# Kernel tuning notes

Measured on AMD Instinct MI355X. Metric: run time of the kernel, lower is better.

## Reference

```python
import jax, jax.numpy as jnp
import numpy as np

INF = 1e10
B, T, D, N, H = 4, 1024, 1024, 16, 4096
SCALE = float(np.sqrt(D))  # Attention built with d_key = d_model in original code


def _linear(x, w, b):
    return x @ w.T + b


def _layernorm(x, gamma, beta, eps=1e-6):
    # torch x.std(-1) is unbiased (ddof=1); eps added to std, matching original
    m = x.mean(-1, keepdims=True)
    var = ((x - m) ** 2).sum(-1, keepdims=True) / (x.shape[-1] - 1)
    return gamma * (x - m) / (jnp.sqrt(var) + eps) + beta


def _mha(q_in, k_in, v_in, wq, bq, wk, bk, wv, bv, wo, bo, mask, causal):
    Bb, Tq, Dm = q_in.shape
    Tk = k_in.shape[1]
    dh = Dm // N
    q = _linear(q_in, wq, bq).reshape(Bb, Tq, N, dh).transpose(0, 2, 1, 3)  # b n q d
    k = _linear(k_in, wk, bk).reshape(Bb, Tk, N, dh).transpose(0, 2, 1, 3)
    v = _linear(v_in, wv, bv).reshape(Bb, Tk, N, dh).transpose(0, 2, 1, 3)
    dots = jnp.einsum('bnqd,bnkd->bnqk', q, k)
    if causal and Tq == Tk:
        tri = jnp.triu(jnp.ones((Tq, Tk), dots.dtype), 1) * INF
        dots = dots - tri
    dots = dots - (1.0 - mask)[:, None, None, :] * INF  # mask: 1=keep
    probs = jax.nn.softmax(dots / SCALE, axis=-1)
    out = jnp.einsum('bnqk,bnkd->bnqd', probs, v)
    out = out.transpose(0, 2, 1, 3).reshape(Bb, Tq, Dm)
    return _linear(out, wo, bo)


def setup_inputs() -> dict:
    key = jax.random.key(0)
    ks = jax.random.split(key, 16)
    g = lambda k, shp: (jax.random.normal(k, shp, dtype=jnp.float32) * 0.02)
    inp = {
        'x': jax.random.normal(ks[0], (B, T, D), dtype=jnp.float32),
        'encoding': jax.random.normal(ks[1], (B, T, D), dtype=jnp.float32),
        'mask_src': jnp.ones((B, T), dtype=jnp.float32),
        'mask_trg': jnp.ones((B, T), dtype=jnp.float32),
        # causal self-attention projections
        'sa_wq': g(ks[2], (D, D)), 'sa_bq': jnp.zeros((D,), jnp.float32),
        'sa_wk': g(ks[3], (D, D)), 'sa_bk': jnp.zeros((D,), jnp.float32),
        'sa_wv': g(ks[4], (D, D)), 'sa_bv': jnp.zeros((D,), jnp.float32),
        'sa_wo': g(ks[5], (D, D)), 'sa_bo': jnp.zeros((D,), jnp.float32),
        'sa_gamma': jnp.ones((D,), jnp.float32), 'sa_beta': jnp.zeros((D,), jnp.float32),
        # cross-attention projections
        'ca_wq': g(ks[6], (D, D)), 'ca_bq': jnp.zeros((D,), jnp.float32),
        'ca_wk': g(ks[7], (D, D)), 'ca_bk': jnp.zeros((D,), jnp.float32),
        'ca_wv': g(ks[8], (D, D)), 'ca_bv': jnp.zeros((D,), jnp.float32),
        'ca_wo': g(ks[9], (D, D)), 'ca_bo': jnp.zeros((D,), jnp.float32),
        'ca_gamma': jnp.ones((D,), jnp.float32), 'ca_beta': jnp.zeros((D,), jnp.float32),
        # feedforward
        'ff_w1': g(ks[10], (H, D)), 'ff_b1': jnp.zeros((H,), jnp.float32),
        'ff_w2': g(ks[11], (D, H)), 'ff_b2': jnp.zeros((D,), jnp.float32),
        'ff_gamma': jnp.ones((D,), jnp.float32), 'ff_beta': jnp.zeros((D,), jnp.float32),
    }
    return inp


def reference(x, encoding, mask_src, mask_trg,
              sa_wq, sa_bq, sa_wk, sa_bk, sa_wv, sa_bv, sa_wo, sa_bo, sa_gamma, sa_beta,
              ca_wq, ca_bq, ca_wk, ca_bk, ca_wv, ca_bv, ca_wo, ca_bo, ca_gamma, ca_beta,
              ff_w1, ff_b1, ff_w2, ff_b2, ff_gamma, ff_beta):
    # DecoderLayer forward (eval: dropout = identity)
    h = _layernorm(x + _mha(x, x, x, sa_wq, sa_bq, sa_wk, sa_bk, sa_wv, sa_bv,
                            sa_wo, sa_bo, mask_trg, causal=True), sa_gamma, sa_beta)
    h = _layernorm(h + _mha(h, encoding, encoding, ca_wq, ca_bq, ca_wk, ca_bk,
                            ca_wv, ca_bv, ca_wo, ca_bo, mask_src, causal=False),
                   ca_gamma, ca_beta)
    ff = _linear(jax.nn.relu(_linear(h, ff_w1, ff_b1)), ff_w2, ff_b2)
    return _layernorm(h + ff, ff_gamma, ff_beta)
```

## Files before the change

kernel.cpp:

```cpp
#include <hip/hip_runtime.h>
#include <hip/hip_bf16.h>
#include <math.h>
#include <stdint.h>

#define BATCH   4
#define TSEQ    1024
#define DMODEL  1024
#define NHEAD   16
#define DHEAD   64
#define HFF     4096
#define MROWS   (BATCH * TSEQ)

typedef _Float16 f16;
typedef __attribute__((ext_vector_type(2))) _Float16 f16x2;
typedef __attribute__((ext_vector_type(4))) _Float16 f16x4;
typedef __attribute__((ext_vector_type(8))) _Float16 f16x8;
typedef __attribute__((ext_vector_type(4))) float    f32x4;

__global__ __launch_bounds__(256)
void cvt_f32_f16(const float* __restrict__ in, f16* __restrict__ out, int n)
{
    const int i = (blockIdx.x * 256 + threadIdx.x) * 8;
    if (i < n) {
        const float4 a = *(const float4*)(in + i);
        const float4 b = *(const float4*)(in + i + 4);
        f16x8 o;
        o[0] = (_Float16)a.x; o[1] = (_Float16)a.y; o[2] = (_Float16)a.z; o[3] = (_Float16)a.w;
        o[4] = (_Float16)b.x; o[5] = (_Float16)b.y; o[6] = (_Float16)b.z; o[7] = (_Float16)b.w;
        *(f16x8*)(out + i) = o;
    }
}

template<int TN, bool RES, bool RELU>
__global__ __launch_bounds__(256, 2)
void hgemm(const f16* __restrict__ A, const f16* __restrict__ Wt,
           const float* __restrict__ bias, const f16* __restrict__ Rm,
           f16* __restrict__ C, int M, int N, int K)
{
    constexpr int TM = 128, TK = 32;
    constexpr int NB = TN / 32;
    constexpr int AISS = (TM * TK) / (256 * 8);
    constexpr int BISS = (TN * TK) / (256 * 8);
    __shared__ alignas(16) f16 As[2][TM * TK];
    __shared__ alignas(16) f16 Bs[2][TN * TK];

    const int t = threadIdx.x, ln = t & 63, wv = t >> 6;
    const int wr = wv >> 1, wc = wv & 1;

    const int gx = gridDim.x;
    const int nbk = gx * gridDim.y;
    const int d  = blockIdx.y * gx + blockIdx.x;
    const int wid = (d & 7) * (nbk >> 3) + (d >> 3);
    const int bx = wid % gx, by = wid / gx;

    const size_t m0 = (size_t)by * TM, n0 = (size_t)bx * TN;

    f32x4 acc[4][NB];
#pragma unroll
    for (int i = 0; i < 4; ++i)
#pragma unroll
        for (int j = 0; j < NB; ++j) acc[i][j] = (f32x4){0.f, 0.f, 0.f, 0.f};

    const f16* Ag = A + (m0 + (t >> 2)) * (size_t)K + (t & 3) * 8;
    const f16* Bg = Wt + (n0 + (t >> 2)) * (size_t)K + (t & 3) * 8;

    auto stage = [&](int buf, int k0) {
#pragma unroll
        for (int i = 0; i < AISS; ++i)
            __builtin_amdgcn_global_load_lds(
                (const __attribute__((address_space(1))) unsigned int*)(Ag + (size_t)(i * 64) * K + k0),
                (__attribute__((address_space(3))) unsigned int*)(&As[buf][(i * 256 + wv * 64) * 8]),
                16, 0, 0);
#pragma unroll
        for (int i = 0; i < BISS; ++i)
            __builtin_amdgcn_global_load_lds(
                (const __attribute__((address_space(1))) unsigned int*)(Bg + (size_t)(i * 64) * K + k0),
                (__attribute__((address_space(3))) unsigned int*)(&Bs[buf][(i * 256 + wv * 64) * 8]),
                16, 0, 0);
    };

    stage(0, 0);
    __syncthreads();
    int buf = 0;
    for (int k0 = 0; k0 < K; k0 += TK) {
        if (k0 + TK < K) stage(buf ^ 1, k0 + TK);
        f16x8 af[4], bf[NB];
        const f16* Ab = As[buf];
        const f16* Bb = Bs[buf];
#pragma unroll
        for (int i = 0; i < 4; ++i)
            af[i] = *(const f16x8*)(Ab + (wr * 64 + i * 16 + (ln & 15)) * TK + (ln >> 4) * 8);
#pragma unroll
        for (int j = 0; j < NB; ++j)
            bf[j] = *(const f16x8*)(Bb + (wc * (TN / 2) + j * 16 + (ln & 15)) * TK + (ln >> 4) * 8);
#pragma unroll
        for (int i = 0; i < 4; ++i)
#pragma unroll
            for (int j = 0; j < NB; ++j)
                acc[i][j] = __builtin_amdgcn_mfma_f32_16x16x32_f16(af[i], bf[j], acc[i][j], 0, 0, 0);
        __syncthreads();
        buf ^= 1;
    }

    const int colbase = (int)n0 + wc * (TN / 2) + (ln & 15);
    const int rowbase = (int)m0 + wr * 64 + (ln >> 4) * 4;
#pragma unroll
    for (int i = 0; i < 4; ++i) {
#pragma unroll
        for (int j = 0; j < NB; ++j) {
            const int col = colbase + j * 16;
            const float bj = bias[col];
#pragma unroll
            for (int r = 0; r < 4; ++r) {
                const int row = rowbase + i * 16 + r;
                float v = acc[i][j][r] + bj;
                if (RES) v += (float)Rm[(size_t)row * N + col];
                if (RELU) v = fmaxf(v, 0.f);
                C[(size_t)row * N + col] = (f16)v;
            }
        }
    }
}

template<bool CAUSAL>
__global__ __launch_bounds__(256, 2)
void attn_mfma(const f16* __restrict__ Qp, int qstr,
               const f16* __restrict__ Kp, int kstr,
               const f16* __restrict__ Vp, int vstr,
               const float* __restrict__ maskp,
               f16* __restrict__ Op)
{
    __shared__ alignas(16) f16 Ks[64 * 64];
    __shared__ alignas(16) f16 Vt[64 * 64];
    __shared__ alignas(16) f16 Ps[4][16 * 64];
    __shared__ alignas(16) float Msk[64];

    const int t = threadIdx.x, l = t & 63, wv = t >> 6;
    const int g = l >> 4, lq = l & 15, a = l & 7;
    const int bh = blockIdx.y, b = bh >> 4, h = bh & 15;
    const int q0 = blockIdx.x * 64;
    const int q0w = q0 + wv * 16;
    const int bT = b * TSEQ;

    f16x8 qf[2];
    {
        const f16* qp = Qp + (size_t)(bT + q0w + lq) * qstr + h * 64 + g * 8;
        qf[0] = *(const f16x8*)(qp);
        qf[1] = *(const f16x8*)(qp + 32);
    }

    f32x4 oacc[4];
#pragma unroll
    for (int i = 0; i < 4; ++i) oacc[i] = (f32x4){0.f, 0.f, 0.f, 0.f};
    float mrun = -1e30f, lrun = 0.f;

    const float* mrow = maskp + b * TSEQ;
    const int kend = CAUSAL ? (q0 + 64) : TSEQ;
    const int qmaxw = q0w + 15;

    f16x8 kr0, kr1, vr0, vr1;
    float mreg = 0.f;
    const int kkey = t >> 3, kd8 = t & 7;

    auto issue_loads = [&](int k0) {
        kr0 = *(const f16x8*)(Kp + (size_t)(bT + k0 + kkey) * kstr + h * 64 + kd8 * 8);
        kr1 = *(const f16x8*)(Kp + (size_t)(bT + k0 + 32 + kkey) * kstr + h * 64 + kd8 * 8);
        vr0 = *(const f16x8*)(Vp + (size_t)(bT + k0 + l) * vstr + h * 64 + wv * 8);
        vr1 = *(const f16x8*)(Vp + (size_t)(bT + k0 + l) * vstr + h * 64 + (4 + wv) * 8);
        if (t < 64) mreg = mrow[k0 + t];
    };
    auto write_stage = [&]() {
        *(f16x8*)&Ks[kkey * 64 + ((kd8 * 8) ^ ((kkey & 7) * 8))] = kr0;
        const int k2 = kkey + 32;
        *(f16x8*)&Ks[k2 * 64 + ((kd8 * 8) ^ ((k2 & 7) * 8))] = kr1;
#pragma unroll
        for (int e = 0; e < 8; ++e) {
            const int d0 = wv * 8 + e;
            const int d1 = (4 + wv) * 8 + e;
            Vt[d0 * 64 + (l ^ (e * 8))] = vr0[e];
            Vt[d1 * 64 + (l ^ (e * 8))] = vr1[e];
        }
        if (t < 64) Msk[t] = mreg;
    };

    issue_loads(0);
    write_stage();
    __syncthreads();

    f16* Pw = Ps[wv];

    for (int k0 = 0; k0 < kend; k0 += 64) {
        const int knext = k0 + 64;
        if (knext < kend) issue_loads(knext);

        if (!CAUSAL || k0 <= qmaxw) {
            f32x4 sacc[4];
#pragma unroll
            for (int kt = 0; kt < 4; ++kt) {
                const int row = kt * 16 + lq;
                const int sw = (row & 7) * 8;
                const f16x8 a0 = *(const f16x8*)&Ks[row * 64 + ((g * 8) ^ sw)];
                const f16x8 a1 = *(const f16x8*)&Ks[row * 64 + (((4 + g) * 8) ^ sw)];
                f32x4 z = (f32x4){0.f, 0.f, 0.f, 0.f};
                z = __builtin_amdgcn_mfma_f32_16x16x32_f16(a0, qf[0], z, 0, 0, 0);
                sacc[kt] = __builtin_amdgcn_mfma_f32_16x16x32_f16(a1, qf[1], z, 0, 0, 0);
            }
            float p[4][4];
            float tmax = -3.0e38f;
#pragma unroll
            for (int kt = 0; kt < 4; ++kt) {
                const float4 mk = *(const float4*)&Msk[kt * 16 + g * 4];
                const float mka[4] = {mk.x, mk.y, mk.z, mk.w};
#pragma unroll
                for (int r = 0; r < 4; ++r) {
                    float s = sacc[kt][r] * (1.f / 32.f) - (1.f - mka[r]) * 3.125e8f;
                    if (CAUSAL) {
                        const int key = k0 + kt * 16 + g * 4 + r;
                        if (key > q0w + lq) s = -3.0e38f;
                    }
                    p[kt][r] = s;
                    tmax = fmaxf(tmax, s);
                }
            }
            tmax = fmaxf(tmax, __shfl_xor(tmax, 16));
            tmax = fmaxf(tmax, __shfl_xor(tmax, 32));
            const float mnew = fmaxf(mrun, tmax);
            const float corr = __expf(mrun - mnew);
            mrun = mnew;
            lrun *= corr;
#pragma unroll
            for (int i = 0; i < 4; ++i) {
                oacc[i][0] *= corr; oacc[i][1] *= corr;
                oacc[i][2] *= corr; oacc[i][3] *= corr;
            }
            float rsum = 0.f;
#pragma unroll
            for (int kt = 0; kt < 4; ++kt)
#pragma unroll
                for (int r = 0; r < 4; ++r) {
                    const float e = __expf(p[kt][r] - mnew);
                    p[kt][r] = e;
                    rsum += e;
                }
            rsum += __shfl_xor(rsum, 16);
            rsum += __shfl_xor(rsum, 32);
            lrun += rsum;
#pragma unroll
            for (int kt = 0; kt < 4; ++kt) {
                f16x4 pv;
                pv[0] = (_Float16)p[kt][0]; pv[1] = (_Float16)p[kt][1];
                pv[2] = (_Float16)p[kt][2]; pv[3] = (_Float16)p[kt][3];
                const int kb = kt * 16 + g * 4;
                *(f16x4*)&Pw[lq * 64 + (kb ^ (a * 8))] = pv;
            }
            const f16x8 pf0 = *(const f16x8*)&Pw[lq * 64 + ((g * 8) ^ (a * 8))];
            const f16x8 pf1 = *(const f16x8*)&Pw[lq * 64 + (((4 + g) * 8) ^ (a * 8))];
#pragma unroll
            for (int dt = 0; dt < 4; ++dt) {
                const int row = dt * 16 + lq;
                const int sw = (row & 7) * 8;
                const f16x8 v0 = *(const f16x8*)&Vt[row * 64 + ((g * 8) ^ sw)];
                const f16x8 v1 = *(const f16x8*)&Vt[row * 64 + (((4 + g) * 8) ^ sw)];
                oacc[dt] = __builtin_amdgcn_mfma_f32_16x16x32_f16(v0, pf0, oacc[dt], 0, 0, 0);
                oacc[dt] = __builtin_amdgcn_mfma_f32_16x16x32_f16(v1, pf1, oacc[dt], 0, 0, 0);
            }
        }

        __syncthreads();
        if (knext < kend) write_stage();
        __syncthreads();
    }

    const float inv = 1.f / lrun;
#pragma unroll
    for (int dt = 0; dt < 4; ++dt) {
        f16x4 ov;
        ov[0] = (_Float16)(oacc[dt][0] * inv); ov[1] = (_Float16)(oacc[dt][1] * inv);
        ov[2] = (_Float16)(oacc[dt][2] * inv); ov[3] = (_Float16)(oacc[dt][3] * inv);
        const int db = dt * 16 + g * 4;
        *(f16x4*)&Pw[lq * 64 + (db ^ (a * 8))] = ov;
    }
#pragma unroll
    for (int i = 0; i < 2; ++i) {
        const int c = i * 64 + l;
        const int row = c >> 3, c8 = c & 7;
        const f16x8 ov = *(const f16x8*)&Pw[row * 64 + ((c8 * 8) ^ ((row & 7) * 8))];
        *(f16x8*)(Op + (size_t)(bT + q0w + row) * DMODEL + h * 64 + c8 * 8) = ov;
    }
}

__inline__ __device__ float block_sum256(float v, float* sm)
{
#pragma unroll
    for (int off = 32; off > 0; off >>= 1) v += __shfl_down(v, off, 64);
    const int lane = threadIdx.x & 63, w = threadIdx.x >> 6;
    if (lane == 0) sm[w] = v;
    __syncthreads();
    const float r = sm[0] + sm[1] + sm[2] + sm[3];
    __syncthreads();
    return r;
}

template<bool F32OUT>
__global__ __launch_bounds__(256)
void ln_kernel(const f16* __restrict__ X, const float* __restrict__ g,
               const float* __restrict__ be, void* __restrict__ Yv)
{
    __shared__ float sm[4];
    const int row = blockIdx.x;
    const size_t base = (size_t)row * DMODEL + threadIdx.x * 4;
    const f16x4 xv = *(const f16x4*)(X + base);
    float x[4] = {(float)xv[0], (float)xv[1], (float)xv[2], (float)xv[3]};

    float s = x[0] + x[1] + x[2] + x[3];
    s = block_sum256(s, sm);
    const float mean = s * (1.0f / (float)DMODEL);

    float dx[4] = {x[0] - mean, x[1] - mean, x[2] - mean, x[3] - mean};
    float s2 = dx[0] * dx[0] + dx[1] * dx[1] + dx[2] * dx[2] + dx[3] * dx[3];
    s2 = block_sum256(s2, sm);
    const float rs = 1.0f / (sqrtf(s2 * (1.0f / (float)(DMODEL - 1))) + 1e-6f);

    const float4 gv = *(const float4*)(g + threadIdx.x * 4);
    const float4 bv = *(const float4*)(be + threadIdx.x * 4);
    const float y0 = gv.x * dx[0] * rs + bv.x;
    const float y1 = gv.y * dx[1] * rs + bv.y;
    const float y2 = gv.z * dx[2] * rs + bv.z;
    const float y3 = gv.w * dx[3] * rs + bv.w;
    if (F32OUT) {
        float4 y = {y0, y1, y2, y3};
        *(float4*)((float*)Yv + base) = y;
    } else {
        f16x4 y; y[0] = (_Float16)y0; y[1] = (_Float16)y1; y[2] = (_Float16)y2; y[3] = (_Float16)y3;
        *(f16x4*)((f16*)Yv + base) = y;
    }
}

extern "C" void kernel_launch(void* const* d_in, const int* in_sizes, int n_in,
                              void* d_out, int out_size, void* d_ws, size_t ws_size,
                              hipStream_t stream)
{
    (void)in_sizes; (void)n_in; (void)out_size; (void)ws_size;

    const float* x        = (const float*)d_in[0];
    const float* enc      = (const float*)d_in[1];
    const float* mask_src = (const float*)d_in[2];
    const float* mask_trg = (const float*)d_in[3];
    const float* sa_wq = (const float*)d_in[4];  const float* sa_bq = (const float*)d_in[5];
    const float* sa_wk = (const float*)d_in[6];  const float* sa_bk = (const float*)d_in[7];
    const float* sa_wv = (const float*)d_in[8];  const float* sa_bv = (const float*)d_in[9];
    const float* sa_wo = (const float*)d_in[10]; const float* sa_bo = (const float*)d_in[11];
    const float* sa_g  = (const float*)d_in[12]; const float* sa_b  = (const float*)d_in[13];
    const float* ca_wq = (const float*)d_in[14]; const float* ca_bq = (const float*)d_in[15];
    const float* ca_wk = (const float*)d_in[16]; const float* ca_bk = (const float*)d_in[17];
    const float* ca_wv = (const float*)d_in[18]; const float* ca_bv = (const float*)d_in[19];
    const float* ca_wo = (const float*)d_in[20]; const float* ca_bo = (const float*)d_in[21];
    const float* ca_g  = (const float*)d_in[22]; const float* ca_b  = (const float*)d_in[23];
    const float* ff_w1 = (const float*)d_in[24]; const float* ff_b1 = (const float*)d_in[25];
    const float* ff_w2 = (const float*)d_in[26]; const float* ff_b2 = (const float*)d_in[27];
    const float* ff_g  = (const float*)d_in[28]; const float* ff_b  = (const float*)d_in[29];

    f16* ws = (f16*)d_ws;
    const size_t MEG = 1024 * 1024;
    f16* Wh = ws;
    f16* G  = ws + 4 * MEG;
    f16* S0 = ws + 20 * MEG;
    f16* S1 = ws + 24 * MEG;
    f16* S2 = ws + 28 * MEG;
    f16* S3 = ws + 32 * MEG;
    f16* S4 = ws + 36 * MEG;
    f16* S5 = ws + 40 * MEG;
    float* Bias = (float*)((char*)d_ws + 88 * MEG);

    const int NACT = MROWS * DMODEL;
    const int NW   = DMODEL * DMODEL;

    dim3 blk(256);
    const int cvAct = NACT / 2048, cvW = NW / 2048, cvFF = (4 * NW) / 2048;
    dim3 gQKV(3072 / 128, MROWS / 128);
    dim3 gN64(DMODEL / 64, MROWS / 128);
    dim3 gKV(2048 / 128, MROWS / 128);
    dim3 gFF1(HFF / 128, MROWS / 128);
    dim3 agrid(TSEQ / 64, BATCH * NHEAD);

    cvt_f32_f16<<<cvAct, blk, 0, stream>>>(x, S0, NACT);
    cvt_f32_f16<<<cvAct, blk, 0, stream>>>(enc, S1, NACT);
    cvt_f32_f16<<<cvW, blk, 0, stream>>>(sa_wq, Wh, NW);
    cvt_f32_f16<<<cvW, blk, 0, stream>>>(sa_wk, Wh + 1 * MEG, NW);
    cvt_f32_f16<<<cvW, blk, 0, stream>>>(sa_wv, Wh + 2 * MEG, NW);
    hipMemcpyAsync(Bias + 0,    sa_bq, 4096, hipMemcpyDeviceToDevice, stream);
    hipMemcpyAsync(Bias + 1024, sa_bk, 4096, hipMemcpyDeviceToDevice, stream);
    hipMemcpyAsync(Bias + 2048, sa_bv, 4096, hipMemcpyDeviceToDevice, stream);
    hgemm<128, false, false><<<gQKV, blk, 0, stream>>>(S0, Wh, Bias, nullptr, G, MROWS, 3072, DMODEL);
    attn_mfma<true><<<agrid, blk, 0, stream>>>(G, 3072, G + 1024, 3072, G + 2048, 3072, mask_trg, S2);
    cvt_f32_f16<<<cvW, blk, 0, stream>>>(sa_wo, Wh, NW);
    hipMemcpyAsync(Bias, sa_bo, 4096, hipMemcpyDeviceToDevice, stream);
    hgemm<64, true, false><<<gN64, blk, 0, stream>>>(S2, Wh, Bias, S0, S3, MROWS, DMODEL, DMODEL);
    ln_kernel<false><<<MROWS, blk, 0, stream>>>(S3, sa_g, sa_b, S4);

    cvt_f32_f16<<<cvW, blk, 0, stream>>>(ca_wq, Wh, NW);
    hipMemcpyAsync(Bias, ca_bq, 4096, hipMemcpyDeviceToDevice, stream);
    hgemm<64, false, false><<<gN64, blk, 0, stream>>>(S4, Wh, Bias, nullptr, G, MROWS, DMODEL, DMODEL);
    cvt_f32_f16<<<cvW, blk, 0, stream>>>(ca_wk, Wh, NW);
    cvt_f32_f16<<<cvW, blk, 0, stream>>>(ca_wv, Wh + 1 * MEG, NW);
    hipMemcpyAsync(Bias + 0,    ca_bk, 4096, hipMemcpyDeviceToDevice, stream);
    hipMemcpyAsync(Bias + 1024, ca_bv, 4096, hipMemcpyDeviceToDevice, stream);
    hgemm<128, false, false><<<gKV, blk, 0, stream>>>(S1, Wh, Bias, nullptr, G + 4 * MEG, MROWS, 2048, DMODEL);
    attn_mfma<false><<<agrid, blk, 0, stream>>>(G, 1024, G + 4 * MEG, 2048, G + 4 * MEG + 1024, 2048, mask_src, S2);
    cvt_f32_f16<<<cvW, blk, 0, stream>>>(ca_wo, Wh, NW);
    hipMemcpyAsync(Bias, ca_bo, 4096, hipMemcpyDeviceToDevice, stream);
    hgemm<64, true, false><<<gN64, blk, 0, stream>>>(S2, Wh, Bias, S4, S3, MROWS, DMODEL, DMODEL);
    ln_kernel<false><<<MROWS, blk, 0, stream>>>(S3, ca_g, ca_b, S5);

    cvt_f32_f16<<<cvFF, blk, 0, stream>>>(ff_w1, Wh, 4 * NW);
    hipMemcpyAsync(Bias, ff_b1, 16384, hipMemcpyDeviceToDevice, stream);
    hgemm<128, false, true><<<gFF1, blk, 0, stream>>>(S5, Wh, Bias, nullptr, G, MROWS, HFF, DMODEL);
    cvt_f32_f16<<<cvFF, blk, 0, stream>>>(ff_w2, Wh, 4 * NW);
    hipMemcpyAsync(Bias, ff_b2, 4096, hipMemcpyDeviceToDevice, stream);
    hgemm<64, true, false><<<gN64, blk, 0, stream>>>(G, Wh, Bias, S5, S3, MROWS, DMODEL, HFF);
    ln_kernel<true><<<MROWS, blk, 0, stream>>>(S3, ff_g, ff_b, d_out);
}
```

Baseline: 581.5 us.

## Batch weight/bias conversion into single kernels and add swizzled TK=64 GEMM

Replaces the many per-weight conversion launches and bias memcpys with one combined f32-to-f16 prep kernel and one bias-gather kernel, cutting launch and serialization overhead. The GEMM gains a templated K-tile (TK=64 for the N=64 GEMMs) with an XOR-swizzled LDS layout to reduce bank conflicts, and takes a leading-dimension argument so attention writes its output in place into the QKV buffer, removing separate scratch buffers. Doubling the K tile raises LDS use, which may lower occupancy.

```diff
diff --git a/kernel.cpp b/kernel.cpp
--- a/kernel.cpp
+++ b/kernel.cpp
@@ -12,35 +12,65 @@
 #define MROWS   (BATCH * TSEQ)
 
 typedef _Float16 f16;
-typedef __attribute__((ext_vector_type(2))) _Float16 f16x2;
 typedef __attribute__((ext_vector_type(4))) _Float16 f16x4;
 typedef __attribute__((ext_vector_type(8))) _Float16 f16x8;
 typedef __attribute__((ext_vector_type(4))) float    f32x4;
 
+#define MEG (1u << 20)
+
+struct WSrcs { const float* p[12]; };
+
 __global__ __launch_bounds__(256)
-void cvt_f32_f16(const float* __restrict__ in, f16* __restrict__ out, int n)
-{
-    const int i = (blockIdx.x * 256 + threadIdx.x) * 8;
-    if (i < n) {
-        const float4 a = *(const float4*)(in + i);
-        const float4 b = *(const float4*)(in + i + 4);
-        f16x8 o;
-        o[0] = (_Float16)a.x; o[1] = (_Float16)a.y; o[2] = (_Float16)a.z; o[3] = (_Float16)a.w;
-        o[4] = (_Float16)b.x; o[5] = (_Float16)b.y; o[6] = (_Float16)b.z; o[7] = (_Float16)b.w;
-        *(f16x8*)(out + i) = o;
-    }
-}
-
-template<int TN, bool RES, bool RELU>
+void prep_w(WSrcs s, f16* __restrict__ wb)
+{
+    const int blk = blockIdx.x;
+    int seg, off;
+    if      (blk <  4096) { seg = blk >> 9; off = blk & 511;  }
+    else if (blk <  6144) { seg = 8;  off = blk - 4096; }
+    else if (blk <  8192) { seg = 9;  off = blk - 6144; }
+    else if (blk < 10240) { seg = 10; off = blk - 8192; }
+    else                  { seg = 11; off = blk - 10240; }
+    const unsigned dsto[12] = {0, 1*MEG, 2*MEG, 3*MEG, 4*MEG, 5*MEG, 6*MEG, 7*MEG,
+                               8*MEG, 12*MEG, 32*MEG, 36*MEG};
+    const int i = off * 2048 + threadIdx.x * 8;
+    const float4 a = *(const float4*)(s.p[seg] + i);
+    const float4 b = *(const float4*)(s.p[seg] + i + 4);
+    f16x8 o;
+    o[0] = (_Float16)a.x; o[1] = (_Float16)a.y; o[2] = (_Float16)a.z; o[3] = (_Float16)a.w;
+    o[4] = (_Float16)b.x; o[5] = (_Float16)b.y; o[6] = (_Float16)b.z; o[7] = (_Float16)b.w;
+    *(f16x8*)(wb + dsto[seg] + i) = o;
+}
+
+struct BSrcs { const float* p[10]; };
+
+__global__ __launch_bounds__(256)
+void prep_b(BSrcs s, float* __restrict__ bias)
+{
+    const int blk = blockIdx.x;
+    int seg, off;
+    if      (blk <  8) { seg = blk; off = 0; }
+    else if (blk < 12) { seg = 8;   off = blk - 8; }
+    else               { seg = 9;   off = 0; }
+    const unsigned dsto[10] = {0, 1024, 2048, 3072, 4096, 5120, 6144, 7168, 8192, 12288};
+    const int i = off * 1024 + threadIdx.x * 4;
+    const float4 v = *(const float4*)(s.p[seg] + i);
+    *(float4*)(bias + dsto[seg] + i) = v;
+}
+
+template<int TN, int TK, bool RES, bool RELU>
 __global__ __launch_bounds__(256, 2)
-void hgemm(const f16* __restrict__ A, const f16* __restrict__ Wt,
-           const float* __restrict__ bias, const f16* __restrict__ Rm,
-           f16* __restrict__ C, int M, int N, int K)
-{
-    constexpr int TM = 128, TK = 32;
+void hgemm(const f16* __restrict__ A, int lda,
+           const f16* __restrict__ Wt, const float* __restrict__ bias,
+           const f16* __restrict__ Rm, f16* __restrict__ C,
+           int M, int N, int K)
+{
+    constexpr int TM = 128;
     constexpr int NB = TN / 32;
-    constexpr int AISS = (TM * TK) / (256 * 8);
-    constexpr int BISS = (TN * TK) / (256 * 8);
+    constexpr int NK = TK / 32;
+    constexpr int CH = TK / 8;
+    constexpr int RPI = 256 / CH;
+    constexpr int AISS = TM / RPI, BISS = TN / RPI;
+    constexpr int KM = CH - 1;
     __shared__ alignas(16) f16 As[2][TM * TK];
     __shared__ alignas(16) f16 Bs[2][TN * TK];
 
@@ -49,10 +79,9 @@
 
     const int gx = gridDim.x;
     const int nbk = gx * gridDim.y;
-    const int d  = blockIdx.y * gx + blockIdx.x;
-    const int wid = (d & 7) * (nbk >> 3) + (d >> 3);
+    const int dd = blockIdx.y * gx + blockIdx.x;
+    const int wid = (dd & 7) * (nbk >> 3) + (dd >> 3);
     const int bx = wid % gx, by = wid / gx;
-
     const size_t m0 = (size_t)by * TM, n0 = (size_t)bx * TN;
 
     f32x4 acc[4][NB];
@@ -61,21 +90,23 @@
 #pragma unroll
         for (int j = 0; j < NB; ++j) acc[i][j] = (f32x4){0.f, 0.f, 0.f, 0.f};
 
-    const f16* Ag = A + (m0 + (t >> 2)) * (size_t)K + (t & 3) * 8;
-    const f16* Bg = Wt + (n0 + (t >> 2)) * (size_t)K + (t & 3) * 8;
+    const int srow = t / CH;
+    const int scol = ((t % CH) ^ (srow & KM)) * 8;
+    const f16* Ag = A + (m0 + srow) * (size_t)lda + scol;
+    const f16* Bg = Wt + (n0 + srow) * (size_t)K + scol;
 
     auto stage = [&](int buf, int k0) {
 #pragma unroll
         for (int i = 0; i < AISS; ++i)
             __builtin_amdgcn_global_load_lds(
-                (const __attribute__((address_space(1))) unsigned int*)(Ag + (size_t)(i * 64) * K + k0),
-                (__attribute__((address_space(3))) unsigned int*)(&As[buf][(i * 256 + wv * 64) * 8]),
+                (const __attribute__((address_space(1))) unsigned int*)(Ag + (size_t)(i * RPI) * lda + k0),
+                (__attribute__((address_space(3))) unsigned int*)(&As[buf][i * RPI * TK + t * 8]),
                 16, 0, 0);
 #pragma unroll
         for (int i = 0; i < BISS; ++i)
             __builtin_amdgcn_global_load_lds(
-                (const __attribute__((address_space(1))) unsigned int*)(Bg + (size_t)(i * 64) * K + k0),
-                (__attribute__((address_space(3))) unsigned int*)(&Bs[buf][(i * 256 + wv * 64) * 8]),
+                (const __attribute__((address_space(1))) unsigned int*)(Bg + (size_t)(i * RPI) * K + k0),
+                (__attribute__((address_space(3))) unsigned int*)(&Bs[buf][i * RPI * TK + t * 8]),
                 16, 0, 0);
     };
 
@@ -84,20 +115,31 @@
     int buf = 0;
     for (int k0 = 0; k0 < K; k0 += TK) {
         if (k0 + TK < K) stage(buf ^ 1, k0 + TK);
-        f16x8 af[4], bf[NB];
+
+        f16x8 af[NK][4], bf[NK][NB];
         const f16* Ab = As[buf];
         const f16* Bb = Bs[buf];
 #pragma unroll
-        for (int i = 0; i < 4; ++i)
-            af[i] = *(const f16x8*)(Ab + (wr * 64 + i * 16 + (ln & 15)) * TK + (ln >> 4) * 8);
-#pragma unroll
-        for (int j = 0; j < NB; ++j)
-            bf[j] = *(const f16x8*)(Bb + (wc * (TN / 2) + j * 16 + (ln & 15)) * TK + (ln >> 4) * 8);
-#pragma unroll
-        for (int i = 0; i < 4; ++i)
-#pragma unroll
-            for (int j = 0; j < NB; ++j)
-                acc[i][j] = __builtin_amdgcn_mfma_f32_16x16x32_f16(af[i], bf[j], acc[i][j], 0, 0, 0);
+        for (int kk = 0; kk < NK; ++kk) {
+            const int c = kk * 4 + (ln >> 4);
+#pragma unroll
+            for (int i = 0; i < 4; ++i) {
+                const int row = wr * 64 + i * 16 + (ln & 15);
+                af[kk][i] = *(const f16x8*)(Ab + row * TK + ((c ^ (row & KM)) * 8));
+            }
+#pragma unroll
+            for (int j = 0; j < NB; ++j) {
+                const int row = wc * (TN / 2) + j * 16 + (ln & 15);
+                bf[kk][j] = *(const f16x8*)(Bb + row * TK + ((c ^ (row & KM)) * 8));
+            }
+        }
+#pragma unroll
+        for (int kk = 0; kk < NK; ++kk)
+#pragma unroll
+            for (int i = 0; i < 4; ++i)
+#pragma unroll
+                for (int j = 0; j < NB; ++j)
+                    acc[i][j] = __builtin_amdgcn_mfma_f32_16x16x32_f16(af[kk][i], bf[kk][j], acc[i][j], 0, 0, 0);
         __syncthreads();
         buf ^= 1;
     }
@@ -128,7 +170,7 @@
                const f16* __restrict__ Kp, int kstr,
                const f16* __restrict__ Vp, int vstr,
                const float* __restrict__ maskp,
-               f16* __restrict__ Op)
+               f16* __restrict__ Op, int ostr)
 {
     __shared__ alignas(16) f16 Ks[64 * 64];
     __shared__ alignas(16) f16 Vt[64 * 64];
@@ -285,7 +327,7 @@
         const int c = i * 64 + l;
         const int row = c >> 3, c8 = c & 7;
         const f16x8 ov = *(const f16x8*)&Pw[row * 64 + ((c8 * 8) ^ ((row & 7) * 8))];
-        *(f16x8*)(Op + (size_t)(bT + q0w + row) * DMODEL + h * 64 + c8 * 8) = ov;
+        *(f16x8*)(Op + (size_t)(bT + q0w + row) * ostr + h * 64 + c8 * 8) = ov;
     }
 }
 
@@ -360,63 +402,50 @@
     const float* ff_w2 = (const float*)d_in[26]; const float* ff_b2 = (const float*)d_in[27];
     const float* ff_g  = (const float*)d_in[28]; const float* ff_b  = (const float*)d_in[29];
 
-    f16* ws = (f16*)d_ws;
-    const size_t MEG = 1024 * 1024;
-    f16* Wh = ws;
-    f16* G  = ws + 4 * MEG;
-    f16* S0 = ws + 20 * MEG;
-    f16* S1 = ws + 24 * MEG;
-    f16* S2 = ws + 28 * MEG;
-    f16* S3 = ws + 32 * MEG;
-    f16* S4 = ws + 36 * MEG;
-    f16* S5 = ws + 40 * MEG;
-    float* Bias = (float*)((char*)d_ws + 88 * MEG);
-
-    const int NACT = MROWS * DMODEL;
-    const int NW   = DMODEL * DMODEL;
+    float* Bias = (float*)d_ws;
+    f16* WB = (f16*)d_ws + 26624;
+    f16* G  = WB + 16 * (size_t)MEG;
+    f16* S0 = WB + 32 * (size_t)MEG;
+    f16* S1 = WB + 36 * (size_t)MEG;
+    f16* S4 = WB + 40 * (size_t)MEG;
+    f16* PreLN = G + 12 * (size_t)MEG;
 
     dim3 blk(256);
-    const int cvAct = NACT / 2048, cvW = NW / 2048, cvFF = (4 * NW) / 2048;
     dim3 gQKV(3072 / 128, MROWS / 128);
-    dim3 gN64(DMODEL / 64, MROWS / 128);
-    dim3 gKV(2048 / 128, MROWS / 128);
-    dim3 gFF1(HFF / 128, MROWS / 128);
+    dim3 gN64(1024 / 64,  MROWS / 128);
+    dim3 gKV (2048 / 128, MROWS / 128);
+    dim3 gFF1(4096 / 128, MROWS / 128);
     dim3 agrid(TSEQ / 64, BATCH * NHEAD);
 
-    cvt_f32_f16<<<cvAct, blk, 0, stream>>>(x, S0, NACT);
-    cvt_f32_f16<<<cvAct, blk, 0, stream>>>(enc, S1, NACT);
-    cvt_f32_f16<<<cvW, blk, 0, stream>>>(sa_wq, Wh, NW);
-    cvt_f32_f16<<<cvW, blk, 0, stream>>>(sa_wk, Wh + 1 * MEG, NW);
-    cvt_f32_f16<<<cvW, blk, 0, stream>>>(sa_wv, Wh + 2 * MEG, NW);
-    hipMemcpyAsync(Bias + 0,    sa_bq, 4096, hipMemcpyDeviceToDevice, stream);
-    hipMemcpyAsync(Bias + 1024, sa_bk, 4096, hipMemcpyDeviceToDevice, stream);
-    hipMemcpyAsync(Bias + 2048, sa_bv, 4096, hipMemcpyDeviceToDevice, stream);
-    hgemm<128, false, false><<<gQKV, blk, 0, stream>>>(S0, Wh, Bias, nullptr, G, MROWS, 3072, DMODEL);
-    attn_mfma<true><<<agrid, blk, 0, stream>>>(G, 3072, G + 1024, 3072, G + 2048, 3072, mask_trg, S2);
-    cvt_f32_f16<<<cvW, blk, 0, stream>>>(sa_wo, Wh, NW);
-    hipMemcpyAsync(Bias, sa_bo, 4096, hipMemcpyDeviceToDevice, stream);
-    hgemm<64, true, false><<<gN64, blk, 0, stream>>>(S2, Wh, Bias, S0, S3, MROWS, DMODEL, DMODEL);
-    ln_kernel<false><<<MROWS, blk, 0, stream>>>(S3, sa_g, sa_b, S4);
-
-    cvt_f32_f16<<<cvW, blk, 0, stream>>>(ca_wq, Wh, NW);
-    hipMemcpyAsync(Bias, ca_bq, 4096, hipMemcpyDeviceToDevice, stream);
-    hgemm<64, false, false><<<gN64, blk, 0, stream>>>(S4, Wh, Bias, nullptr, G, MROWS, DMODEL, DMODEL);
-    cvt_f32_f16<<<cvW, blk, 0, stream>>>(ca_wk, Wh, NW);
-    cvt_f32_f16<<<cvW, blk, 0, stream>>>(ca_wv, Wh + 1 * MEG, NW);
-    hipMemcpyAsync(Bias + 0,    ca_bk, 4096, hipMemcpyDeviceToDevice, stream);
-    hipMemcpyAsync(Bias + 1024, ca_bv, 4096, hipMemcpyDeviceToDevice, stream);
-    hgemm<128, false, false><<<gKV, blk, 0, stream>>>(S1, Wh, Bias, nullptr, G + 4 * MEG, MROWS, 2048, DMODEL);
-    attn_mfma<false><<<agrid, blk, 0, stream>>>(G, 1024, G + 4 * MEG, 2048, G + 4 * MEG + 1024, 2048, mask_src, S2);
-    cvt_f32_f16<<<cvW, blk, 0, stream>>>(ca_wo, Wh, NW);
-    hipMemcpyAsync(Bias, ca_bo, 4096, hipMemcpyDeviceToDevice, stream);
-    hgemm<64, true, false><<<gN64, blk, 0, stream>>>(S2, Wh, Bias, S4, S3, MROWS, DMODEL, DMODEL);
-    ln_kernel<false><<<MROWS, blk, 0, stream>>>(S3, ca_g, ca_b, S5);
-
-    cvt_f32_f16<<<cvFF, blk, 0, stream>>>(ff_w1, Wh, 4 * NW);
-    hipMemcpyAsync(Bias, ff_b1, 16384, hipMemcpyDeviceToDevice, stream);
-    hgemm<128, false, true><<<gFF1, blk, 0, stream>>>(S5, Wh, Bias, nullptr, G, MROWS, HFF, DMODEL);
-    cvt_f32_f16<<<cvFF, blk, 0, stream>>>(ff_w2, Wh, 4 * NW);
-    hipMemcpyAsync(Bias, ff_b2, 4096, hipMemcpyDeviceToDevice, stream);
-    hgemm<64, true, false><<<gN64, blk, 0, stream>>>(G, Wh, Bias, S5, S3, MROWS, DMODEL, HFF);
-    ln_kernel<true><<<MROWS, blk, 0, stream>>>(S3, ff_g, ff_b, d_out);
-}
+    WSrcs wsrc = {{sa_wq, sa_wk, sa_wv, sa_wo, ca_wq, ca_wk, ca_wv, ca_wo,
+                   ff_w1, ff_w2, x, enc}};
+    prep_w<<<12288, blk, 0, stream>>>(wsrc, WB);
+    BSrcs bsrc = {{sa_bq, sa_bk, sa_bv, sa_bo, ca_bq, ca_bk, ca_bv, ca_bo,
+                   ff_b1, ff_b2}};
+    prep_b<<<13, blk, 0, stream>>>(bsrc, Bias);
+
+    hgemm<128, 32, false, false><<<gQKV, blk, 0, stream>>>(
+        S0, DMODEL, WB, Bias, nullptr, G, MROWS, 3072, DMODEL);
+    attn_mfma<true><<<agrid, blk, 0, stream>>>(
+        G, 3072, G + 1024, 3072, G + 2048, 3072, mask_trg, G, 3072);
+    hgemm<64, 64, true, false><<<gN64, blk, 0, stream>>>(
+        G, 3072, WB + 3 * (size_t)MEG, Bias + 3072, S0, PreLN, MROWS, DMODEL, DMODEL);
+    ln_kernel<false><<<MROWS, blk, 0, stream>>>(PreLN, sa_g, sa_b, S4);
+
+    hgemm<64, 64, false, false><<<gN64, blk, 0, stream>>>(
+        S4, DMODEL, WB + 4 * (size_t)MEG, Bias + 4096, nullptr, G, MROWS, DMODEL, DMODEL);
+    hgemm<128, 32, false, false><<<gKV, blk, 0, stream>>>(
+        S1, DMODEL, WB + 5 * (size_t)MEG, Bias + 5120, nullptr, G + 4 * (size_t)MEG,
+        MROWS, 2048, DMODEL);
+    attn_mfma<false><<<agrid, blk, 0, stream>>>(
+        G, 1024, G + 4 * (size_t)MEG, 2048, G + 4 * (size_t)MEG + 1024, 2048, mask_src, G, 1024);
+    hgemm<64, 64, true, false><<<gN64, blk, 0, stream>>>(
+        G, 1024, WB + 7 * (size_t)MEG, Bias + 7168, S4, PreLN, MROWS, DMODEL, DMODEL);
+    ln_kernel<false><<<MROWS, blk, 0, stream>>>(PreLN, ca_g, ca_b, S4);
+
+    hgemm<128, 32, false, true><<<gFF1, blk, 0, stream>>>(
+        S4, DMODEL, WB + 8 * (size_t)MEG, Bias + 8192, nullptr, G, MROWS, HFF, DMODEL);
+    hgemm<64, 64, true, false><<<gN64, blk, 0, stream>>>(
+        G, HFF, WB + 12 * (size_t)MEG, Bias + 12288, S4, S0, MROWS, DMODEL, HFF);
+    ln_kernel<true><<<MROWS, blk, 0, stream>>>(S0, ff_g, ff_b, d_out);
+}
```

After: 516.7 us. 1.13x faster.
